# Optimization experiments

Hardware: AMD Instinct MI355X
Metric: run time of the kernel (lower is better)

## Reference

```python
import jax, jax.numpy as jnp
import numpy as np

B, H, W, C = 32, 32, 32, 256


def setup_inputs() -> dict:
    key = jax.random.key(0)
    k1, k2 = jax.random.split(key)
    feats1 = jax.random.normal(k1, (B, H, W, C), dtype=jnp.float32)
    feats2 = jax.random.normal(k2, (B, H, W, C), dtype=jnp.float32)
    return {"feats1": feats1, "feats2": feats2}


def reference(feats1, feats2):
    # Training path of LocalFeatureLoss (trainflag=True)
    b, h, w, c = feats1.shape
    l = h * w
    q = feats1.reshape(b, l, c)  # queries: (B, l, C)
    p = feats2.reshape(b, l, c)  # preds:   (B, l, C)
    # M[b, a, j] = <p[b,a], q[b,j]>  == fm2 @ fm1.T per batch
    M = jnp.einsum('bac,bjc->baj', p, q)  # (B, l_pred, l_query)
    max1 = jnp.argmax(M, axis=1)  # (B, l_q): best pred index for each query token
    max2 = jnp.argmax(M, axis=2)  # (B, l_p): best query index for each pred token
    # mutual nearest-neighbor check: m[b, j] = max2[b, max1[b, j]]
    m = jnp.take_along_axis(max2, max1, axis=1)  # (B, l_q)
    valid = jnp.arange(l)[None, :] == m          # (B, l_q) bool
    # gather matched pred descriptors and compute per-pair similarity
    matched_p = jnp.take_along_axis(p, max1[..., None], axis=1)  # (B, l_q, C)
    sims = jnp.sum(q * matched_p, axis=-1)                        # (B, l_q)
    cnt = jnp.sum(valid, axis=1).astype(sims.dtype)               # (B,)
    # mean over mutual NN pairs (torch mean over idx1)
    similarity = jnp.sum(jnp.where(valid, sims, 0.0), axis=1) / jnp.maximum(cnt, 1.0)
    return similarity
```

## Files before the change

### kernel.cpp

```cpp
#include <hip/hip_runtime.h>
#include <hip/hip_bf16.h>

#define BATCH 32
#define L 1024
#define CD 256
#define TM 64
#define TN 64
#define NT (L / TN)
#define KC 128
#define RT_PER_B 16
#define SP_LD (CD + 8)
#define SQ_LD (KC + 8)

typedef __bf16 bf16x8 __attribute__((ext_vector_type(8)));
typedef __bf16 bf16x4 __attribute__((ext_vector_type(4)));
typedef float  f32x4  __attribute__((ext_vector_type(4)));

__device__ __forceinline__ unsigned int enc_f32(float f) {
    unsigned int u = __float_as_uint(f);
    return ((int)u < 0) ? ~u : (u | 0x80000000u);
}
__device__ __forceinline__ float dec_f32(unsigned int u) {
    u = (u & 0x80000000u) ? (u & 0x7FFFFFFFu) : ~u;
    return __uint_as_float(u);
}
__device__ __forceinline__ unsigned long long pmax(unsigned long long a, unsigned long long b) {
    return a > b ? a : b;
}
__device__ __forceinline__ bf16x4 cvt4(float4 v) {
    bf16x4 o;
    o[0] = (__bf16)v.x; o[1] = (__bf16)v.y; o[2] = (__bf16)v.z; o[3] = (__bf16)v.w;
    return o;
}

__global__ __launch_bounds__(256) void mm_argmax_kernel(
    const float* __restrict__ qg,
    const float* __restrict__ pg,
    unsigned long long* __restrict__ colpart,
    int* __restrict__ max2)
{
    __shared__ __bf16 sP[TM][SP_LD];
    __shared__ __bf16 sQ[TN][SQ_LD];
    __shared__ unsigned long long sCol[TN];
    __shared__ unsigned long long sRowW[2][TM];

    const int tid = threadIdx.x;
    const int bid = blockIdx.x;
    const int b    = bid & 31;
    const int rt   = bid >> 5;
    const int row0 = rt * TM;

    const int lane = tid & 63;
    const int w    = tid >> 6;
    const int wm   = w >> 1;
    const int wn   = w & 1;
    const int quad = lane >> 4;
    const int l16  = lane & 15;

    const float* pB = pg + ((size_t)b * L + row0) * CD;
    const float* qB = qg + (size_t)b * L * CD;

    const int sr = tid >> 2;
    const int sc = tid & 3;
    {
        const float4* src = (const float4*)(pB + sr * CD);
        #pragma unroll
        for (int i = 0; i < 16; ++i)
            *(bf16x4*)&sP[sr][(sc + i * 4) * 4] = cvt4(src[sc + i * 4]);
    }

    float4 pf[8];
    {
        const float4* src = (const float4*)(qB + (size_t)sr * CD);
        #pragma unroll
        for (int i = 0; i < 8; ++i) pf[i] = src[sc + i * 4];
    }

    unsigned long long rowbest[2][4];
    #pragma unroll
    for (int tm = 0; tm < 2; ++tm)
        #pragma unroll
        for (int r = 0; r < 4; ++r) rowbest[tm][r] = 0ull;
    unsigned long long pend[2] = {0ull, 0ull};

    for (int nt = 0; nt < NT; ++nt) {
        f32x4 acc[2][2];
        #pragma unroll
        for (int tm = 0; tm < 2; ++tm)
            #pragma unroll
            for (int tn = 0; tn < 2; ++tn) acc[tm][tn] = (f32x4){0.f, 0.f, 0.f, 0.f};

        for (int kc = 0; kc < 2; ++kc) {
            if (nt || kc) __syncthreads();
            if (kc == 0 && nt > 0 && wm == 1 && quad == 0) {
                #pragma unroll
                for (int tn = 0; tn < 2; ++tn) {
                    const int c = wn * 32 + tn * 16 + l16;
                    colpart[((size_t)b * RT_PER_B + rt) * L + (nt - 1) * TN + c] =
                        pmax(pend[tn], sCol[c]);
                }
            }
            #pragma unroll
            for (int i = 0; i < 8; ++i)
                *(bf16x4*)&sQ[sr][(sc + i * 4) * 4] = cvt4(pf[i]);
            if (!(nt == NT - 1 && kc == 1)) {
                const int nnt = (kc == 0) ? nt : nt + 1;
                const int nkc = kc ^ 1;
                const float4* src = (const float4*)(qB + (size_t)(nnt * TN + sr) * CD + nkc * KC);
                #pragma unroll
                for (int i = 0; i < 8; ++i) pf[i] = src[sc + i * 4];
            }
            __syncthreads();
            #pragma unroll
            for (int kk = 0; kk < 4; ++kk) {
                const int ka = kc * KC + kk * 32 + quad * 8;
                const int kb = kk * 32 + quad * 8;
                bf16x8 a0 = *(const bf16x8*)&sP[wm * 32 +      l16][ka];
                bf16x8 a1 = *(const bf16x8*)&sP[wm * 32 + 16 + l16][ka];
                bf16x8 b0 = *(const bf16x8*)&sQ[wn * 32 +      l16][kb];
                bf16x8 b1 = *(const bf16x8*)&sQ[wn * 32 + 16 + l16][kb];
                acc[0][0] = __builtin_amdgcn_mfma_f32_16x16x32_bf16(a0, b0, acc[0][0], 0, 0, 0);
                acc[0][1] = __builtin_amdgcn_mfma_f32_16x16x32_bf16(a0, b1, acc[0][1], 0, 0, 0);
                acc[1][0] = __builtin_amdgcn_mfma_f32_16x16x32_bf16(a1, b0, acc[1][0], 0, 0, 0);
                acc[1][1] = __builtin_amdgcn_mfma_f32_16x16x32_bf16(a1, b1, acc[1][1], 0, 0, 0);
            }
        }

        #pragma unroll
        for (int tn = 0; tn < 2; ++tn) {
            const unsigned int jcol = (unsigned int)(nt * TN + wn * 32 + tn * 16 + l16);
            const unsigned long long jpk = (unsigned long long)(unsigned int)(~jcol);
            unsigned long long cbest = 0ull;
            #pragma unroll
            for (int tm = 0; tm < 2; ++tm) {
                #pragma unroll
                for (int r = 0; r < 4; ++r) {
                    const unsigned int e = enc_f32(acc[tm][tn][r]);
                    const unsigned int aidx =
                        (unsigned int)(row0 + wm * 32 + tm * 16 + quad * 4 + r);
                    cbest = pmax(cbest, ((unsigned long long)e << 32) | (unsigned int)(~aidx));
                    rowbest[tm][r] = pmax(rowbest[tm][r], ((unsigned long long)e << 32) | jpk);
                }
            }
            cbest = pmax(cbest, __shfl_xor(cbest, 16));
            cbest = pmax(cbest, __shfl_xor(cbest, 32));
            if (quad == 0) {
                const int c = wn * 32 + tn * 16 + l16;
                if (wm == 0) sCol[c] = cbest;
                else         pend[tn] = cbest;
            }
        }
    }

    __syncthreads();
    if (wm == 1 && quad == 0) {
        #pragma unroll
        for (int tn = 0; tn < 2; ++tn) {
            const int c = wn * 32 + tn * 16 + l16;
            colpart[((size_t)b * RT_PER_B + rt) * L + (NT - 1) * TN + c] =
                pmax(pend[tn], sCol[c]);
        }
    }

    #pragma unroll
    for (int tm = 0; tm < 2; ++tm) {
        #pragma unroll
        for (int r = 0; r < 4; ++r) {
            unsigned long long pk = rowbest[tm][r];
            pk = pmax(pk, __shfl_xor(pk, 1));
            pk = pmax(pk, __shfl_xor(pk, 2));
            pk = pmax(pk, __shfl_xor(pk, 4));
            pk = pmax(pk, __shfl_xor(pk, 8));
            rowbest[tm][r] = pk;
        }
    }
    if (l16 == 0) {
        #pragma unroll
        for (int tm = 0; tm < 2; ++tm)
            #pragma unroll
            for (int r = 0; r < 4; ++r)
                sRowW[wn][wm * 32 + tm * 16 + quad * 4 + r] = rowbest[tm][r];
    }
    __syncthreads();
    if (w == 0) {
        unsigned long long m = pmax(sRowW[0][lane], sRowW[1][lane]);
        max2[(size_t)b * L + row0 + lane] = (int)(~(unsigned int)m);
    }
}

__global__ __launch_bounds__(256) void finalize_kernel(
    const unsigned long long* __restrict__ colpart,
    const int* __restrict__ max2,
    float* __restrict__ out)
{
    __shared__ int sMax2[L];
    __shared__ float sSum[4];
    __shared__ int sCnt[4];
    const int b = blockIdx.x;
    const int tid = threadIdx.x;

    for (int i = tid; i < L; i += 256) sMax2[i] = max2[(size_t)b * L + i];
    __syncthreads();

    float sum = 0.f;
    int cnt = 0;
    #pragma unroll
    for (int i = 0; i < 4; ++i) {
        const int j = tid + i * 256;
        unsigned long long best = 0ull;
        #pragma unroll
        for (int rt = 0; rt < RT_PER_B; ++rt)
            best = pmax(best, colpart[((size_t)b * RT_PER_B + rt) * L + j]);
        const int a = (int)(~(unsigned int)best) & (L - 1);
        const float val = dec_f32((unsigned int)(best >> 32));
        if (sMax2[a] == j) { sum += val; ++cnt; }
    }
    #pragma unroll
    for (int o = 32; o >= 1; o >>= 1) {
        sum += __shfl_down(sum, o);
        cnt += __shfl_down(cnt, o);
    }
    if ((tid & 63) == 0) { sSum[tid >> 6] = sum; sCnt[tid >> 6] = cnt; }
    __syncthreads();
    if (tid == 0) {
        float S = sSum[0] + sSum[1] + sSum[2] + sSum[3];
        int   C = sCnt[0] + sCnt[1] + sCnt[2] + sCnt[3];
        out[b] = S / fmaxf((float)C, 1.0f);
    }
}

extern "C" void kernel_launch(void* const* d_in, const int* in_sizes, int n_in,
                              void* d_out, int out_size, void* d_ws, size_t ws_size,
                              hipStream_t stream) {
    const float* q = (const float*)d_in[0];
    const float* p = (const float*)d_in[1];
    float* out = (float*)d_out;

    unsigned long long* colpart = (unsigned long long*)d_ws;
    int* max2 = (int*)((char*)d_ws + (size_t)BATCH * RT_PER_B * L * sizeof(unsigned long long));

    mm_argmax_kernel<<<BATCH * RT_PER_B, 256, 0, stream>>>(q, p, colpart, max2);
    finalize_kernel<<<BATCH, 256, 0, stream>>>(colpart, max2, out);
}
```

Before: 135.9 us.

## Use 2D 128x128 output tiles with swizzled LDS and add a partial-argmax reduce kernel

```diff
diff --git a/kernel.cpp b/kernel.cpp
--- a/kernel.cpp
+++ b/kernel.cpp
@@ -4,13 +4,11 @@
 #define BATCH 32
 #define L 1024
 #define CD 256
-#define TM 64
-#define TN 64
-#define NT (L / TN)
-#define KC 128
-#define RT_PER_B 16
-#define SP_LD (CD + 8)
-#define SQ_LD (KC + 8)
+#define BM 128
+#define BN 128
+#define BK 64
+#define NRT (L / BM)
+#define NCT (L / BN)
 
 typedef __bf16 bf16x8 __attribute__((ext_vector_type(8)));
 typedef __bf16 bf16x4 __attribute__((ext_vector_type(4)));
@@ -33,22 +31,25 @@
     return o;
 }
 
-__global__ __launch_bounds__(256) void mm_argmax_kernel(
+__global__ __launch_bounds__(512, 4) void mm_argmax_kernel(
     const float* __restrict__ qg,
     const float* __restrict__ pg,
     unsigned long long* __restrict__ colpart,
-    int* __restrict__ max2)
+    unsigned long long* __restrict__ rowpart)
 {
-    __shared__ __bf16 sP[TM][SP_LD];
-    __shared__ __bf16 sQ[TN][SQ_LD];
-    __shared__ unsigned long long sCol[TN];
-    __shared__ unsigned long long sRowW[2][TM];
+    __shared__ __bf16 sA[BM * BK];
+    __shared__ __bf16 sB[BN * BK];
+    __shared__ unsigned long long sRow[2][BM];
+    __shared__ unsigned long long sCol[4][BN];
 
     const int tid = threadIdx.x;
     const int bid = blockIdx.x;
     const int b    = bid & 31;
-    const int rt   = bid >> 5;
-    const int row0 = rt * TM;
+    const int tile = bid >> 5;
+    const int rt   = tile >> 3;
+    const int ct   = tile & 7;
+    const int row0 = rt * BM;
+    const int col0 = ct * BN;
 
     const int lane = tid & 63;
     const int w    = tid >> 6;
@@ -57,139 +58,141 @@
     const int quad = lane >> 4;
     const int l16  = lane & 15;
 
-    const float* pB = pg + ((size_t)b * L + row0) * CD;
-    const float* qB = qg + (size_t)b * L * CD;
-
-    const int sr = tid >> 2;
-    const int sc = tid & 3;
-    {
-        const float4* src = (const float4*)(pB + sr * CD);
-        #pragma unroll
-        for (int i = 0; i < 16; ++i)
-            *(bf16x4*)&sP[sr][(sc + i * 4) * 4] = cvt4(src[sc + i * 4]);
-    }
-
-    float4 pf[8];
-    {
-        const float4* src = (const float4*)(qB + (size_t)sr * CD);
-        #pragma unroll
-        for (int i = 0; i < 8; ++i) pf[i] = src[sc + i * 4];
-    }
-
-    unsigned long long rowbest[2][4];
+    const float* pA = pg + ((size_t)b * L + row0) * CD;
+    const float* pB = qg + ((size_t)b * L + col0) * CD;
+
+    const int sr = tid >> 4;
+    const int sl = tid & 15;
+
+    f32x4 acc[2][4];
     #pragma unroll
     for (int tm = 0; tm < 2; ++tm)
         #pragma unroll
-        for (int r = 0; r < 4; ++r) rowbest[tm][r] = 0ull;
-    unsigned long long pend[2] = {0ull, 0ull};
-
-    for (int nt = 0; nt < NT; ++nt) {
-        f32x4 acc[2][2];
+        for (int tn = 0; tn < 4; ++tn) acc[tm][tn] = (f32x4){0.f, 0.f, 0.f, 0.f};
+
+    float4 pfA[4], pfB[4];
+    #pragma unroll
+    for (int p = 0; p < 4; ++p) {
+        pfA[p] = *(const float4*)(pA + (size_t)(p * 32 + sr) * CD + sl * 4);
+        pfB[p] = *(const float4*)(pB + (size_t)(p * 32 + sr) * CD + sl * 4);
+    }
+
+    for (int step = 0; step < 4; ++step) {
+        if (step) __syncthreads();
+        #pragma unroll
+        for (int p = 0; p < 4; ++p) {
+            const int row = p * 32 + sr;
+            const int idx = row * BK + (((sl >> 1) ^ (row & 7)) << 3) + ((sl & 1) << 2);
+            *(bf16x4*)&sA[idx] = cvt4(pfA[p]);
+            *(bf16x4*)&sB[idx] = cvt4(pfB[p]);
+        }
+        if (step < 3) {
+            const int k0 = (step + 1) * BK;
+            #pragma unroll
+            for (int p = 0; p < 4; ++p) {
+                pfA[p] = *(const float4*)(pA + (size_t)(p * 32 + sr) * CD + k0 + sl * 4);
+                pfB[p] = *(const float4*)(pB + (size_t)(p * 32 + sr) * CD + k0 + sl * 4);
+            }
+        }
+        __syncthreads();
+        #pragma unroll
+        for (int kk = 0; kk < 2; ++kk) {
+            const int sw = ((kk * 4 + quad) ^ (l16 & 7)) << 3;
+            bf16x8 a0 = *(const bf16x8*)&sA[(wm * 32      + l16) * BK + sw];
+            bf16x8 a1 = *(const bf16x8*)&sA[(wm * 32 + 16 + l16) * BK + sw];
+            bf16x8 b0 = *(const bf16x8*)&sB[(wn * 64      + l16) * BK + sw];
+            bf16x8 b1 = *(const bf16x8*)&sB[(wn * 64 + 16 + l16) * BK + sw];
+            bf16x8 b2 = *(const bf16x8*)&sB[(wn * 64 + 32 + l16) * BK + sw];
+            bf16x8 b3 = *(const bf16x8*)&sB[(wn * 64 + 48 + l16) * BK + sw];
+            acc[0][0] = __builtin_amdgcn_mfma_f32_16x16x32_bf16(a0, b0, acc[0][0], 0, 0, 0);
+            acc[0][1] = __builtin_amdgcn_mfma_f32_16x16x32_bf16(a0, b1, acc[0][1], 0, 0, 0);
+            acc[0][2] = __builtin_amdgcn_mfma_f32_16x16x32_bf16(a0, b2, acc[0][2], 0, 0, 0);
+            acc[0][3] = __builtin_amdgcn_mfma_f32_16x16x32_bf16(a0, b3, acc[0][3], 0, 0, 0);
+            acc[1][0] = __builtin_amdgcn_mfma_f32_16x16x32_bf16(a1, b0, acc[1][0], 0, 0, 0);
+            acc[1][1] = __builtin_amdgcn_mfma_f32_16x16x32_bf16(a1, b1, acc[1][1], 0, 0, 0);
+            acc[1][2] = __builtin_amdgcn_mfma_f32_16x16x32_bf16(a1, b2, acc[1][2], 0, 0, 0);
+            acc[1][3] = __builtin_amdgcn_mfma_f32_16x16x32_bf16(a1, b3, acc[1][3], 0, 0, 0);
+        }
+    }
+
+    const int a_base = row0 + wm * 32 + quad * 4;
+    const int j_base = col0 + wn * 64 + l16;
+
+    #pragma unroll
+    for (int tn = 0; tn < 4; ++tn) {
+        float cv = acc[0][tn][0];
+        int   ca = a_base;
         #pragma unroll
         for (int tm = 0; tm < 2; ++tm)
             #pragma unroll
-            for (int tn = 0; tn < 2; ++tn) acc[tm][tn] = (f32x4){0.f, 0.f, 0.f, 0.f};
-
-        for (int kc = 0; kc < 2; ++kc) {
-            if (nt || kc) __syncthreads();
-            if (kc == 0 && nt > 0 && wm == 1 && quad == 0) {
-                #pragma unroll
-                for (int tn = 0; tn < 2; ++tn) {
-                    const int c = wn * 32 + tn * 16 + l16;
-                    colpart[((size_t)b * RT_PER_B + rt) * L + (nt - 1) * TN + c] =
-                        pmax(pend[tn], sCol[c]);
-                }
+            for (int r = 0; r < 4; ++r) {
+                if (tm == 0 && r == 0) continue;
+                const float v = acc[tm][tn][r];
+                const int   a = a_base + tm * 16 + r;
+                if (v > cv) { cv = v; ca = a; }
             }
+        unsigned long long pk =
+            ((unsigned long long)enc_f32(cv) << 32) | (unsigned int)(~(unsigned int)ca);
+        pk = pmax(pk, __shfl_xor(pk, 16));
+        pk = pmax(pk, __shfl_xor(pk, 32));
+        if (quad == 0) sCol[wm][wn * 64 + tn * 16 + l16] = pk;
+    }
+
+    #pragma unroll
+    for (int tm = 0; tm < 2; ++tm)
+        #pragma unroll
+        for (int r = 0; r < 4; ++r) {
+            float rv = acc[tm][0][r];
+            int   rj = j_base;
             #pragma unroll
-            for (int i = 0; i < 8; ++i)
-                *(bf16x4*)&sQ[sr][(sc + i * 4) * 4] = cvt4(pf[i]);
-            if (!(nt == NT - 1 && kc == 1)) {
-                const int nnt = (kc == 0) ? nt : nt + 1;
-                const int nkc = kc ^ 1;
-                const float4* src = (const float4*)(qB + (size_t)(nnt * TN + sr) * CD + nkc * KC);
-                #pragma unroll
-                for (int i = 0; i < 8; ++i) pf[i] = src[sc + i * 4];
+            for (int tn = 1; tn < 4; ++tn) {
+                const float v = acc[tm][tn][r];
+                if (v > rv) { rv = v; rj = j_base + tn * 16; }
             }
-            __syncthreads();
-            #pragma unroll
-            for (int kk = 0; kk < 4; ++kk) {
-                const int ka = kc * KC + kk * 32 + quad * 8;
-                const int kb = kk * 32 + quad * 8;
-                bf16x8 a0 = *(const bf16x8*)&sP[wm * 32 +      l16][ka];
-                bf16x8 a1 = *(const bf16x8*)&sP[wm * 32 + 16 + l16][ka];
-                bf16x8 b0 = *(const bf16x8*)&sQ[wn * 32 +      l16][kb];
-                bf16x8 b1 = *(const bf16x8*)&sQ[wn * 32 + 16 + l16][kb];
-                acc[0][0] = __builtin_amdgcn_mfma_f32_16x16x32_bf16(a0, b0, acc[0][0], 0, 0, 0);
-                acc[0][1] = __builtin_amdgcn_mfma_f32_16x16x32_bf16(a0, b1, acc[0][1], 0, 0, 0);
-                acc[1][0] = __builtin_amdgcn_mfma_f32_16x16x32_bf16(a1, b0, acc[1][0], 0, 0, 0);
-                acc[1][1] = __builtin_amdgcn_mfma_f32_16x16x32_bf16(a1, b1, acc[1][1], 0, 0, 0);
-            }
-        }
-
-        #pragma unroll
-        for (int tn = 0; tn < 2; ++tn) {
-            const unsigned int jcol = (unsigned int)(nt * TN + wn * 32 + tn * 16 + l16);
-            const unsigned long long jpk = (unsigned long long)(unsigned int)(~jcol);
-            unsigned long long cbest = 0ull;
-            #pragma unroll
-            for (int tm = 0; tm < 2; ++tm) {
-                #pragma unroll
-                for (int r = 0; r < 4; ++r) {
-                    const unsigned int e = enc_f32(acc[tm][tn][r]);
-                    const unsigned int aidx =
-                        (unsigned int)(row0 + wm * 32 + tm * 16 + quad * 4 + r);
-                    cbest = pmax(cbest, ((unsigned long long)e << 32) | (unsigned int)(~aidx));
-                    rowbest[tm][r] = pmax(rowbest[tm][r], ((unsigned long long)e << 32) | jpk);
-                }
-            }
-            cbest = pmax(cbest, __shfl_xor(cbest, 16));
-            cbest = pmax(cbest, __shfl_xor(cbest, 32));
-            if (quad == 0) {
-                const int c = wn * 32 + tn * 16 + l16;
-                if (wm == 0) sCol[c] = cbest;
-                else         pend[tn] = cbest;
-            }
-        }
-    }
-
-    __syncthreads();
-    if (wm == 1 && quad == 0) {
-        #pragma unroll
-        for (int tn = 0; tn < 2; ++tn) {
-            const int c = wn * 32 + tn * 16 + l16;
-            colpart[((size_t)b * RT_PER_B + rt) * L + (NT - 1) * TN + c] =
-                pmax(pend[tn], sCol[c]);
-        }
-    }
-
-    #pragma unroll
-    for (int tm = 0; tm < 2; ++tm) {
-        #pragma unroll
-        for (int r = 0; r < 4; ++r) {
-            unsigned long long pk = rowbest[tm][r];
+            unsigned long long pk =
+                ((unsigned long long)enc_f32(rv) << 32) | (unsigned int)(~(unsigned int)rj);
             pk = pmax(pk, __shfl_xor(pk, 1));
             pk = pmax(pk, __shfl_xor(pk, 2));
             pk = pmax(pk, __shfl_xor(pk, 4));
             pk = pmax(pk, __shfl_xor(pk, 8));
-            rowbest[tm][r] = pk;
-        }
-    }
-    if (l16 == 0) {
-        #pragma unroll
-        for (int tm = 0; tm < 2; ++tm)
-            #pragma unroll
-            for (int r = 0; r < 4; ++r)
-                sRowW[wn][wm * 32 + tm * 16 + quad * 4 + r] = rowbest[tm][r];
-    }
+            if (l16 == 0) sRow[wn][wm * 32 + tm * 16 + quad * 4 + r] = pk;
+        }
+
     __syncthreads();
-    if (w == 0) {
-        unsigned long long m = pmax(sRowW[0][lane], sRowW[1][lane]);
-        max2[(size_t)b * L + row0 + lane] = (int)(~(unsigned int)m);
-    }
+    if (tid < BN) {
+        unsigned long long c = pmax(pmax(sCol[0][tid], sCol[1][tid]),
+                                    pmax(sCol[2][tid], sCol[3][tid]));
+        colpart[((size_t)b * NRT + rt) * L + col0 + tid] = c;
+        unsigned long long rr = pmax(sRow[0][tid], sRow[1][tid]);
+        rowpart[((size_t)b * NCT + ct) * L + row0 + tid] = rr;
+    }
+}
+
+__global__ __launch_bounds__(256) void reduce_kernel(
+    const unsigned long long* __restrict__ colpart,
+    const unsigned long long* __restrict__ rowpart,
+    unsigned long long* __restrict__ bestc,
+    int* __restrict__ max2)
+{
+    const int b   = blockIdx.x & 31;
+    const int ch  = blockIdx.x >> 5;
+    const int idx = ch * 256 + threadIdx.x;
+
+    unsigned long long cb = 0ull;
+    #pragma unroll
+    for (int rt = 0; rt < NRT; ++rt)
+        cb = pmax(cb, colpart[((size_t)b * NRT + rt) * L + idx]);
+    bestc[(size_t)b * L + idx] = cb;
+
+    unsigned long long rb = 0ull;
+    #pragma unroll
+    for (int ct = 0; ct < NCT; ++ct)
+        rb = pmax(rb, rowpart[((size_t)b * NCT + ct) * L + idx]);
+    max2[(size_t)b * L + idx] = (int)(~(unsigned int)rb) & (L - 1);
 }
 
 __global__ __launch_bounds__(256) void finalize_kernel(
-    const unsigned long long* __restrict__ colpart,
+    const unsigned long long* __restrict__ bestc,
     const int* __restrict__ max2,
     float* __restrict__ out)
 {
@@ -207,10 +210,7 @@
     #pragma unroll
     for (int i = 0; i < 4; ++i) {
         const int j = tid + i * 256;
-        unsigned long long best = 0ull;
-        #pragma unroll
-        for (int rt = 0; rt < RT_PER_B; ++rt)
-            best = pmax(best, colpart[((size_t)b * RT_PER_B + rt) * L + j]);
+        const unsigned long long best = bestc[(size_t)b * L + j];
         const int a = (int)(~(unsigned int)best) & (L - 1);
         const float val = dec_f32((unsigned int)(best >> 32));
         if (sMax2[a] == j) { sum += val; ++cnt; }
@@ -237,8 +237,11 @@
     float* out = (float*)d_out;
 
     unsigned long long* colpart = (unsigned long long*)d_ws;
-    int* max2 = (int*)((char*)d_ws + (size_t)BATCH * RT_PER_B * L * sizeof(unsigned long long));
-
-    mm_argmax_kernel<<<BATCH * RT_PER_B, 256, 0, stream>>>(q, p, colpart, max2);
-    finalize_kernel<<<BATCH, 256, 0, stream>>>(colpart, max2, out);
-}
+    unsigned long long* rowpart = colpart + (size_t)BATCH * NRT * L;
+    unsigned long long* bestc   = rowpart + (size_t)BATCH * NCT * L;
+    int* max2 = (int*)(bestc + (size_t)BATCH * L);
+
+    mm_argmax_kernel<<<BATCH * NRT * NCT, 512, 0, stream>>>(q, p, colpart, rowpart);
+    reduce_kernel<<<BATCH * 4, 256, 0, stream>>>(colpart, rowpart, bestc, max2);
+    finalize_kernel<<<BATCH, 256, 0, stream>>>(bestc, max2, out);
+}
```

Result: no change. 137.0 us (+0.8%).
